# Kernel optimization log

Measured on AMD Instinct MI355X. Metric: run time of the kernel, lower is better.

## Reference

```python
import jax, jax.numpy as jnp
import numpy as np

B, L = 64, 1024
ENC_DIM, DEC_DIM, ATT_DIM = 512, 512, 512


def setup_inputs() -> dict:
    key = jax.random.key(0)
    ks = jax.random.split(key, 11)
    s_enc = 1.0 / np.sqrt(ENC_DIM)
    s_dec = 1.0 / np.sqrt(DEC_DIM)
    s_att = 1.0 / np.sqrt(ATT_DIM)
    return {
        "encoder_features": jax.random.normal(ks[0], (B, L, ENC_DIM), jnp.float32),
        "decoder_hidden": jax.random.normal(ks[1], (B, DEC_DIM), jnp.float32),
        "coverage": jax.random.uniform(ks[2], (B, L), jnp.float32),
        # nn.Linear params (torch stores weight as [out, in]; we keep [in, out])
        "W_enc": jax.random.uniform(ks[3], (ENC_DIM, ATT_DIM), jnp.float32, -s_enc, s_enc),
        "b_enc": jax.random.uniform(ks[4], (ATT_DIM,), jnp.float32, -s_enc, s_enc),
        "W_dec": jax.random.uniform(ks[5], (DEC_DIM, ATT_DIM), jnp.float32, -s_dec, s_dec),
        "b_dec": jax.random.uniform(ks[6], (ATT_DIM,), jnp.float32, -s_dec, s_dec),
        "W_cov": jax.random.uniform(ks[7], (1, ATT_DIM), jnp.float32, -1.0, 1.0),
        "b_cov": jax.random.uniform(ks[8], (ATT_DIM,), jnp.float32, -1.0, 1.0),
        "W_full": jax.random.uniform(ks[9], (ATT_DIM, 1), jnp.float32, -s_att, s_att),
        "b_full": jax.random.uniform(ks[10], (1,), jnp.float32, -s_att, s_att),
    }


def reference(encoder_features, decoder_hidden, coverage,
              W_enc, b_enc, W_dec, b_dec, W_cov, b_cov, W_full, b_full):
    # att1: [B, L, A]
    att1 = jnp.einsum("ble,ea->bla", encoder_features, W_enc) + b_enc
    # att2: [B, 1, A]
    att2 = (decoder_hidden @ W_dec + b_dec)[:, None, :]
    # att3: coverage[B,L] through Linear(1, A) -> outer product, [B, L, A]
    att3 = coverage[:, :, None] * W_cov[0] + b_cov
    # energy: [B, L]
    energy = (jax.nn.relu(att1 + att2 + att3) @ W_full)[:, :, 0] + b_full[0]
    alpha = jax.nn.softmax(energy, axis=1)  # [B, L]
    new_coverage = coverage + alpha
    attention_weighted_encoding = jnp.einsum("ble,bl->be", encoder_features, alpha)
    return (attention_weighted_encoding, alpha, new_coverage)
```

## Files before the change

kernel.cpp:

```cpp
#include <hip/hip_runtime.h>
#include <cstdint>
#include <cstddef>

#define NB   64
#define NL   1024
#define NA   512
#define NE   512
#define NROWS (NB*NL)

typedef __attribute__((ext_vector_type(8))) short bf16x8;
typedef __attribute__((ext_vector_type(4))) float f32x4;

__device__ __forceinline__ unsigned short f2bf(float x){
    unsigned int u = __float_as_uint(x);
    u += 0x7FFFu + ((u >> 16) & 1u);
    return (unsigned short)(u >> 16);
}

__global__ __launch_bounds__(256) void k_wfrag(const float* __restrict__ Wenc,
                                               unsigned short* __restrict__ wfrag){
    const int g    = blockIdx.x * 256 + threadIdx.x;
    const int lane = g & 63;
    const int n    = (g >> 6) & 31;
    const int ks   = (g >> 11) & 1;
    const int s    = g >> 12;
    const int col  = n * 16 + (lane & 15);
    const int kb   = s * 64 + ks * 32 + (lane >> 4) * 8;
    unsigned int w[4];
    #pragma unroll
    for (int p = 0; p < 4; ++p){
        unsigned short lo = f2bf(Wenc[(size_t)(kb + 2*p    ) * NA + col]);
        unsigned short hi = f2bf(Wenc[(size_t)(kb + 2*p + 1) * NA + col]);
        w[p] = (unsigned int)lo | ((unsigned int)hi << 16);
    }
    ((uint4*)wfrag)[g] = make_uint4(w[0], w[1], w[2], w[3]);
}

__global__ __launch_bounds__(256) void k_base(const float* __restrict__ dh,
                                              const float* __restrict__ Wdec,
                                              const float* __restrict__ bdec,
                                              const float* __restrict__ benc,
                                              const float* __restrict__ bcov,
                                              float* __restrict__ base){
    const int b   = blockIdx.x >> 3;
    const int a0  = (blockIdx.x & 7) * 64;
    const int tid = threadIdx.x;
    const int al  = tid & 63, kg = tid >> 6;
    __shared__ float h[512];
    __shared__ float ps[4][64];
    h[tid]       = dh[b * 512 + tid];
    h[tid + 256] = dh[b * 512 + tid + 256];
    __syncthreads();
    const float* wp = Wdec + (size_t)(kg * 128) * 512 + a0 + al;
    const float* hp = h + kg * 128;
    float s0 = 0.f, s1 = 0.f, s2 = 0.f, s3 = 0.f;
    #pragma unroll
    for (int k = 0; k < 128; k += 4){
        s0 += hp[k + 0] * wp[(size_t)(k + 0) * 512];
        s1 += hp[k + 1] * wp[(size_t)(k + 1) * 512];
        s2 += hp[k + 2] * wp[(size_t)(k + 2) * 512];
        s3 += hp[k + 3] * wp[(size_t)(k + 3) * 512];
    }
    ps[kg][al] = (s0 + s1) + (s2 + s3);
    __syncthreads();
    if (tid < 64){
        const int a = a0 + tid;
        base[b * 512 + a] = ps[0][tid] + ps[1][tid] + ps[2][tid] + ps[3][tid]
                          + bdec[a] + benc[a] + bcov[a];
    }
}

__global__ __launch_bounds__(256, 2) void k_energy(
        const float* __restrict__ enc,
        const float* __restrict__ cov,
        const float* __restrict__ base,
        const unsigned short* __restrict__ wfrag,
        const float* __restrict__ Wcov,
        const float* __restrict__ Wfull,
        float* __restrict__ energy)
{
    __shared__ __align__(16) unsigned char sB[65536];
    __shared__ __align__(16) unsigned char sA[8192];
    __shared__ float sCov[64];
    __shared__ float sEp[4][64];

    const int tid  = threadIdx.x;
    const int wid  = tid >> 6, lane = tid & 63;
    const int r0   = blockIdx.x * 64;
    const int b    = r0 >> 10;

    if (tid < 64) sCov[tid] = cov[r0 + tid];

    f32x4 acc[4][8];
    #pragma unroll
    for (int m = 0; m < 4; ++m)
        #pragma unroll
        for (int n = 0; n < 8; ++n) acc[m][n] = (f32x4){0.f, 0.f, 0.f, 0.f};

    const int rloc = tid >> 2, q = tid & 3;
    const float* arow = enc + (size_t)(r0 + rloc) * NE + q * 16;
    unsigned char* aw = sA + (((q >> 1) * 4 + (rloc >> 4)) * 1024
                              + ((rloc & 15) + 32 * (q & 1)) * 16);
    const unsigned char* bsrc = (const unsigned char*)wfrag + wid * 16384 + lane * 16;
    unsigned char* bdst = sB + wid * 16384;

    for (int s = 0; s < 8; ++s){
        __syncthreads();
        const unsigned char* bs = bsrc + (size_t)s * 65536;
        #pragma unroll
        for (int i = 0; i < 16; ++i){
            __builtin_amdgcn_global_load_lds(
                (__attribute__((address_space(1))) void*)(bs + i * 1024),
                (__attribute__((address_space(3))) void*)(bdst + i * 1024),
                16, 0, 0);
        }
        const float* ap = arow + s * 64;
        float4 v0 = *(const float4*)(ap);
        float4 v1 = *(const float4*)(ap + 4);
        float4 v2 = *(const float4*)(ap + 8);
        float4 v3 = *(const float4*)(ap + 12);
        uint4 f1, f2;
        f1.x = f2bf(v0.x) | ((unsigned)f2bf(v0.y) << 16);
        f1.y = f2bf(v0.z) | ((unsigned)f2bf(v0.w) << 16);
        f1.z = f2bf(v1.x) | ((unsigned)f2bf(v1.y) << 16);
        f1.w = f2bf(v1.z) | ((unsigned)f2bf(v1.w) << 16);
        f2.x = f2bf(v2.x) | ((unsigned)f2bf(v2.y) << 16);
        f2.y = f2bf(v2.z) | ((unsigned)f2bf(v2.w) << 16);
        f2.z = f2bf(v3.x) | ((unsigned)f2bf(v3.y) << 16);
        f2.w = f2bf(v3.z) | ((unsigned)f2bf(v3.w) << 16);
        *(uint4*)(aw)       = f1;
        *(uint4*)(aw + 256) = f2;
        __syncthreads();
        bf16x8 af[2][4];
        #pragma unroll
        for (int ks = 0; ks < 2; ++ks)
            #pragma unroll
            for (int m = 0; m < 4; ++m)
                af[ks][m] = *(const bf16x8*)(sA + (ks*4 + m) * 1024 + lane * 16);
        #pragma unroll
        for (int ks = 0; ks < 2; ++ks){
            #pragma unroll
            for (int n = 0; n < 8; ++n){
                bf16x8 bfr = *(const bf16x8*)(sB + (ks*32 + wid*8 + n) * 1024 + lane * 16);
                #pragma unroll
                for (int m = 0; m < 4; ++m)
                    acc[m][n] = __builtin_amdgcn_mfma_f32_16x16x32_bf16(
                                    af[ks][m], bfr, acc[m][n], 0, 0, 0);
            }
        }
    }

    const int c0 = wid * 128 + (lane & 15);
    float basev[8], wcovv[8], wfullv[8];
    #pragma unroll
    for (int n = 0; n < 8; ++n){
        const int c = c0 + n * 16;
        basev[n]  = base[b * 512 + c];
        wcovv[n]  = Wcov[c];
        wfullv[n] = Wfull[c];
    }
    const int hi = lane >> 4;
    float covr[4][4];
    #pragma unroll
    for (int m = 0; m < 4; ++m)
        #pragma unroll
        for (int r = 0; r < 4; ++r) covr[m][r] = sCov[m*16 + 4*hi + r];
    float epv[4][4] = {};
    #pragma unroll
    for (int m = 0; m < 4; ++m)
        #pragma unroll
        for (int n = 0; n < 8; ++n)
            #pragma unroll
            for (int r = 0; r < 4; ++r){
                float v = acc[m][n][r] + basev[n] + covr[m][r] * wcovv[n];
                v = fmaxf(v, 0.f);
                epv[m][r] += v * wfullv[n];
            }
    #pragma unroll
    for (int m = 0; m < 4; ++m)
        #pragma unroll
        for (int r = 0; r < 4; ++r){
            float v = epv[m][r];
            v += __shfl_xor(v, 1);
            v += __shfl_xor(v, 2);
            v += __shfl_xor(v, 4);
            v += __shfl_xor(v, 8);
            epv[m][r] = v;
        }
    if ((lane & 15) == 0){
        #pragma unroll
        for (int m = 0; m < 4; ++m)
            #pragma unroll
            for (int r = 0; r < 4; ++r)
                sEp[wid][m*16 + 4*hi + r] = epv[m][r];
    }
    __syncthreads();
    if (tid < 64)
        energy[r0 + tid] = sEp[0][tid] + sEp[1][tid] + sEp[2][tid] + sEp[3][tid];
}

#define AWE_OFF   0
#define ALPHA_OFF 32768
#define NCOV_OFF  98304

__global__ __launch_bounds__(256) void k_finish(
        const float* __restrict__ enc, const float* __restrict__ cov,
        const float* __restrict__ energy, float* __restrict__ out)
{
    const int bid = blockIdx.x;
    const int b = bid >> 3, ec = bid & 7;
    const int tid = threadIdx.x;
    __shared__ float sa[1024];
    __shared__ float rb[16];
    __shared__ float ps[4][64];

    float4 ev = ((const float4*)(energy + b * 1024))[tid];
    float mx = fmaxf(fmaxf(ev.x, ev.y), fmaxf(ev.z, ev.w));
    #pragma unroll
    for (int off = 32; off; off >>= 1) mx = fmaxf(mx, __shfl_xor(mx, off));
    if ((tid & 63) == 0) rb[tid >> 6] = mx;
    __syncthreads();
    mx = fmaxf(fmaxf(rb[0], rb[1]), fmaxf(rb[2], rb[3]));
    float e0 = __expf(ev.x - mx), e1 = __expf(ev.y - mx),
          e2 = __expf(ev.z - mx), e3 = __expf(ev.w - mx);
    ((float4*)sa)[tid] = make_float4(e0, e1, e2, e3);
    float sm = e0 + e1 + e2 + e3;
    #pragma unroll
    for (int off = 32; off; off >>= 1) sm += __shfl_xor(sm, off);
    if ((tid & 63) == 0) rb[8 + (tid >> 6)] = sm;
    __syncthreads();
    const float inv = 1.0f / (rb[8] + rb[9] + rb[10] + rb[11]);

    if (ec == 0){
        #pragma unroll
        for (int i = 0; i < 4; ++i){
            const int idx = tid + i * 256;
            const float a = sa[idx] * inv;
            out[ALPHA_OFF + b * 1024 + idx] = a;
            out[NCOV_OFF  + b * 1024 + idx] = cov[b * 1024 + idx] + a;
        }
    }

    const int qt = tid >> 6, cl = tid & 63;
    const float* ep = enc + ((size_t)(b * 1024 + qt * 256)) * 512 + ec * 64 + cl;
    const float* w = sa + qt * 256;
    float a0 = 0.f, a1 = 0.f, a2 = 0.f, a3 = 0.f;
    for (int l = 0; l < 256; l += 4){
        a0 += ep[(size_t)(l + 0) * 512] * w[l + 0];
        a1 += ep[(size_t)(l + 1) * 512] * w[l + 1];
        a2 += ep[(size_t)(l + 2) * 512] * w[l + 2];
        a3 += ep[(size_t)(l + 3) * 512] * w[l + 3];
    }
    ps[qt][cl] = (a0 + a1) + (a2 + a3);
    __syncthreads();
    if (tid < 64)
        out[AWE_OFF + b * 512 + ec * 64 + tid] =
            (ps[0][tid] + ps[1][tid] + ps[2][tid] + ps[3][tid]) * inv;
}

extern "C" void kernel_launch(void* const* d_in, const int* in_sizes, int n_in,
                              void* d_out, int out_size, void* d_ws, size_t ws_size,
                              hipStream_t stream){
    const float* enc   = (const float*)d_in[0];
    const float* dh    = (const float*)d_in[1];
    const float* cov   = (const float*)d_in[2];
    const float* Wenc  = (const float*)d_in[3];
    const float* benc  = (const float*)d_in[4];
    const float* Wdec  = (const float*)d_in[5];
    const float* bdec  = (const float*)d_in[6];
    const float* Wcov  = (const float*)d_in[7];
    const float* bcov  = (const float*)d_in[8];
    const float* Wfull = (const float*)d_in[9];
    float* out = (float*)d_out;

    unsigned short* wfrag = (unsigned short*)d_ws;
    float* base   = (float*)((char*)d_ws + 512 * 1024);
    float* energy = (float*)((char*)d_ws + 640 * 1024);

    k_wfrag <<<128,  256, 0, stream>>>(Wenc, wfrag);
    k_base  <<<512,  256, 0, stream>>>(dh, Wdec, bdec, benc, bcov, base);
    k_energy<<<1024, 256, 0, stream>>>(enc, cov, base, wfrag, Wcov, Wfull, energy);
    k_finish<<<512,  256, 0, stream>>>(enc, cov, energy, out);
}
```

Before: 85.16 us.

## Merge prep kernels, reorder W fragment layout, vectorize weighted-sum loads

```diff
diff --git a/kernel.cpp b/kernel.cpp
--- a/kernel.cpp
+++ b/kernel.cpp
@@ -6,7 +6,6 @@
 #define NL   1024
 #define NA   512
 #define NE   512
-#define NROWS (NB*NL)
 
 typedef __attribute__((ext_vector_type(8))) short bf16x8;
 typedef __attribute__((ext_vector_type(4))) float f32x4;
@@ -17,56 +16,59 @@
     return (unsigned short)(u >> 16);
 }
 
-__global__ __launch_bounds__(256) void k_wfrag(const float* __restrict__ Wenc,
-                                               unsigned short* __restrict__ wfrag){
-    const int g    = blockIdx.x * 256 + threadIdx.x;
-    const int lane = g & 63;
-    const int n    = (g >> 6) & 31;
-    const int ks   = (g >> 11) & 1;
-    const int s    = g >> 12;
-    const int col  = n * 16 + (lane & 15);
-    const int kb   = s * 64 + ks * 32 + (lane >> 4) * 8;
-    unsigned int w[4];
-    #pragma unroll
-    for (int p = 0; p < 4; ++p){
-        unsigned short lo = f2bf(Wenc[(size_t)(kb + 2*p    ) * NA + col]);
-        unsigned short hi = f2bf(Wenc[(size_t)(kb + 2*p + 1) * NA + col]);
-        w[p] = (unsigned int)lo | ((unsigned int)hi << 16);
-    }
-    ((uint4*)wfrag)[g] = make_uint4(w[0], w[1], w[2], w[3]);
-}
-
-__global__ __launch_bounds__(256) void k_base(const float* __restrict__ dh,
+__global__ __launch_bounds__(256) void k_prep(const float* __restrict__ Wenc,
+                                              unsigned short* __restrict__ wfrag,
+                                              const float* __restrict__ dh,
                                               const float* __restrict__ Wdec,
                                               const float* __restrict__ bdec,
                                               const float* __restrict__ benc,
                                               const float* __restrict__ bcov,
                                               float* __restrict__ base){
-    const int b   = blockIdx.x >> 3;
-    const int a0  = (blockIdx.x & 7) * 64;
-    const int tid = threadIdx.x;
-    const int al  = tid & 63, kg = tid >> 6;
-    __shared__ float h[512];
-    __shared__ float ps[4][64];
-    h[tid]       = dh[b * 512 + tid];
-    h[tid + 256] = dh[b * 512 + tid + 256];
-    __syncthreads();
-    const float* wp = Wdec + (size_t)(kg * 128) * 512 + a0 + al;
-    const float* hp = h + kg * 128;
-    float s0 = 0.f, s1 = 0.f, s2 = 0.f, s3 = 0.f;
-    #pragma unroll
-    for (int k = 0; k < 128; k += 4){
-        s0 += hp[k + 0] * wp[(size_t)(k + 0) * 512];
-        s1 += hp[k + 1] * wp[(size_t)(k + 1) * 512];
-        s2 += hp[k + 2] * wp[(size_t)(k + 2) * 512];
-        s3 += hp[k + 3] * wp[(size_t)(k + 3) * 512];
-    }
-    ps[kg][al] = (s0 + s1) + (s2 + s3);
-    __syncthreads();
-    if (tid < 64){
-        const int a = a0 + tid;
-        base[b * 512 + a] = ps[0][tid] + ps[1][tid] + ps[2][tid] + ps[3][tid]
-                          + bdec[a] + benc[a] + bcov[a];
+    const int bid = blockIdx.x, tid = threadIdx.x;
+    if (bid < 128){
+        const int g    = bid * 256 + tid;
+        const int lane = g & 63;
+        const int n    = (g >> 6) & 3;
+        const int ks   = (g >> 8) & 1;
+        const int cw   = (g >> 9) & 7;
+        const int s    = g >> 12;
+        const int col  = cw * 64 + n * 16 + (lane & 15);
+        const int kb   = s * 64 + ks * 32 + (lane >> 4) * 8;
+        unsigned int w[4];
+        #pragma unroll
+        for (int p = 0; p < 4; ++p){
+            unsigned short lo = f2bf(Wenc[(size_t)(kb + 2*p    ) * NA + col]);
+            unsigned short hi = f2bf(Wenc[(size_t)(kb + 2*p + 1) * NA + col]);
+            w[p] = (unsigned int)lo | ((unsigned int)hi << 16);
+        }
+        ((uint4*)wfrag)[g] = make_uint4(w[0], w[1], w[2], w[3]);
+    } else {
+        const int idx = bid - 128;
+        const int b   = idx >> 3;
+        const int a0  = (idx & 7) * 64;
+        const int al  = tid & 63, kg = tid >> 6;
+        __shared__ float h[512];
+        __shared__ float ps[4][64];
+        h[tid]       = dh[b * 512 + tid];
+        h[tid + 256] = dh[b * 512 + tid + 256];
+        __syncthreads();
+        const float* wp = Wdec + (size_t)(kg * 128) * 512 + a0 + al;
+        const float* hp = h + kg * 128;
+        float s0 = 0.f, s1 = 0.f, s2 = 0.f, s3 = 0.f;
+        #pragma unroll
+        for (int k = 0; k < 128; k += 4){
+            s0 += hp[k + 0] * wp[(size_t)(k + 0) * 512];
+            s1 += hp[k + 1] * wp[(size_t)(k + 1) * 512];
+            s2 += hp[k + 2] * wp[(size_t)(k + 2) * 512];
+            s3 += hp[k + 3] * wp[(size_t)(k + 3) * 512];
+        }
+        ps[kg][al] = (s0 + s1) + (s2 + s3);
+        __syncthreads();
+        if (tid < 64){
+            const int a = a0 + tid;
+            base[b * 512 + a] = ps[0][tid] + ps[1][tid] + ps[2][tid] + ps[3][tid]
+                              + bdec[a] + benc[a] + bcov[a];
+        }
     }
 }
 
@@ -141,7 +143,8 @@
         for (int ks = 0; ks < 2; ++ks){
             #pragma unroll
             for (int n = 0; n < 8; ++n){
-                bf16x8 bfr = *(const bf16x8*)(sB + (ks*32 + wid*8 + n) * 1024 + lane * 16);
+                bf16x8 bfr = *(const bf16x8*)(sB
+                    + ((wid*2 + (n>>2)) * 512 + ks * 256 + (n&3) * 64 + lane) * 16);
                 #pragma unroll
                 for (int m = 0; m < 4; ++m)
                     acc[m][n] = __builtin_amdgcn_mfma_f32_16x16x32_bf16(
@@ -154,7 +157,7 @@
     float basev[8], wcovv[8], wfullv[8];
     #pragma unroll
     for (int n = 0; n < 8; ++n){
-        const int c = c0 + n * 16;
+        const int c = c0 + ((n >> 2) * 64) + (n & 3) * 16;
         basev[n]  = base[b * 512 + c];
         wcovv[n]  = Wcov[c];
         wfullv[n] = Wfull[c];
@@ -212,7 +215,7 @@
     const int tid = threadIdx.x;
     __shared__ float sa[1024];
     __shared__ float rb[16];
-    __shared__ float ps[4][64];
+    __shared__ float ps2[16][64];
 
     float4 ev = ((const float4*)(energy + b * 1024))[tid];
     float mx = fmaxf(fmaxf(ev.x, ev.y), fmaxf(ev.z, ev.w));
@@ -241,21 +244,28 @@
         }
     }
 
-    const int qt = tid >> 6, cl = tid & 63;
-    const float* ep = enc + ((size_t)(b * 1024 + qt * 256)) * 512 + ec * 64 + cl;
-    const float* w = sa + qt * 256;
-    float a0 = 0.f, a1 = 0.f, a2 = 0.f, a3 = 0.f;
-    for (int l = 0; l < 256; l += 4){
-        a0 += ep[(size_t)(l + 0) * 512] * w[l + 0];
-        a1 += ep[(size_t)(l + 1) * 512] * w[l + 1];
-        a2 += ep[(size_t)(l + 2) * 512] * w[l + 2];
-        a3 += ep[(size_t)(l + 3) * 512] * w[l + 3];
-    }
-    ps[qt][cl] = (a0 + a1) + (a2 + a3);
-    __syncthreads();
-    if (tid < 64)
-        out[AWE_OFF + b * 512 + ec * 64 + tid] =
-            (ps[0][tid] + ps[1][tid] + ps[2][tid] + ps[3][tid]) * inv;
+    const int cg = tid & 15, rg = tid >> 4;
+    const float4* ep = (const float4*)(enc + (size_t)(b * 1024 + rg * 64) * 512)
+                     + ec * 16 + cg;
+    const float* w = sa + rg * 64;
+    float ax = 0.f, ay = 0.f, az = 0.f, aw = 0.f;
+    #pragma unroll 8
+    for (int l = 0; l < 64; ++l){
+        float4 e4 = ep[(size_t)l * 128];
+        const float wl = w[l];
+        ax += e4.x * wl; ay += e4.y * wl; az += e4.z * wl; aw += e4.w * wl;
+    }
+    ps2[rg][cg * 4 + 0] = ax;
+    ps2[rg][cg * 4 + 1] = ay;
+    ps2[rg][cg * 4 + 2] = az;
+    ps2[rg][cg * 4 + 3] = aw;
+    __syncthreads();
+    if (tid < 64){
+        float s = 0.f;
+        #pragma unroll
+        for (int g = 0; g < 16; ++g) s += ps2[g][tid];
+        out[AWE_OFF + b * 512 + ec * 64 + tid] = s * inv;
+    }
 }
 
 extern "C" void kernel_launch(void* const* d_in, const int* in_sizes, int n_in,
@@ -277,8 +287,7 @@
     float* base   = (float*)((char*)d_ws + 512 * 1024);
     float* energy = (float*)((char*)d_ws + 640 * 1024);
 
-    k_wfrag <<<128,  256, 0, stream>>>(Wenc, wfrag);
-    k_base  <<<512,  256, 0, stream>>>(dh, Wdec, bdec, benc, bcov, base);
+    k_prep  <<<640,  256, 0, stream>>>(Wenc, wfrag, dh, Wdec, bdec, benc, bcov, base);
     k_energy<<<1024, 256, 0, stream>>>(enc, cov, base, wfrag, Wcov, Wfull, energy);
     k_finish<<<512,  256, 0, stream>>>(enc, cov, energy, out);
 }
```

Measured after the change: 82.07 us. 3.6% less time.
